# Kernel tuning notes

Measured on AMD Instinct MI355X. Metric: run time of the kernel, lower is better.

The kernel has to match this reference:

```python
import jax, jax.numpy as jnp
import numpy as np

B, T, TM = 4, 1024, 1500
D_MODEL, D_FFN, H, D_HEAD, D_MEM = 1024, 4096, 16, 64, 1024
EPS = 1e-5


def layernorm(x, g):
    m = jnp.mean(x, axis=-1, keepdims=True)
    xc = x - m
    v = jnp.mean(xc * xc, axis=-1, keepdims=True)
    return xc * jax.lax.rsqrt(v + EPS) * g


def setup_inputs() -> dict:
    key = jax.random.key(0)
    ks = jax.random.split(key, 12)
    s = lambda fan_in: 1.0 / np.sqrt(fan_in)
    return {
        "x": jax.random.normal(ks[0], (B, T, D_MODEL), jnp.float32),
        "encoder_output": jax.random.normal(ks[1], (B, TM, D_MEM), jnp.float32),
        "encoder_mask": jax.random.randint(ks[2], (B, TM), 0, 2).astype(bool),
        "w_qkv": jax.random.normal(ks[3], (D_MODEL, 3 * H * D_HEAD), jnp.float32) * s(D_MODEL),
        "w_o_sa": jax.random.normal(ks[4], (H * D_HEAD, D_MODEL), jnp.float32) * s(H * D_HEAD),
        "w_q": jax.random.normal(ks[5], (D_MODEL, H * D_HEAD), jnp.float32) * s(D_MODEL),
        "w_kv": jax.random.normal(ks[6], (D_MEM, 2 * H * D_HEAD), jnp.float32) * s(D_MEM),
        "w_o_xa": jax.random.normal(ks[7], (H * D_HEAD, D_MODEL), jnp.float32) * s(H * D_HEAD),
        "w_ff1": jax.random.normal(ks[8], (D_MODEL, D_FFN), jnp.float32) * s(D_MODEL),
        "w_ff2": jax.random.normal(ks[9], (D_FFN, D_MODEL), jnp.float32) * s(D_FFN),
        "g_sa": jnp.ones((D_MODEL,), jnp.float32),
        "g_xaq": jnp.ones((D_MODEL,), jnp.float32),
        "g_xam": jnp.ones((D_MEM,), jnp.float32),
        "g_ff": jnp.ones((D_MODEL,), jnp.float32),
    }


def reference(x, encoder_output, encoder_mask, w_qkv, w_o_sa, w_q, w_kv, w_o_xa,
              w_ff1, w_ff2, g_sa, g_xaq, g_xam, g_ff):
    b, t, _ = x.shape
    scale = D_HEAD ** -0.5

    # ---- causal self-attention ----
    residual = x
    xn = layernorm(x, g_sa)
    qkv = (xn @ w_qkv).reshape(b, t, 3, H, D_HEAD)
    q, k, v = qkv[:, :, 0], qkv[:, :, 1], qkv[:, :, 2]  # (B,T,H,D)
    scores = jnp.einsum('bqhd,bkhd->bhqk', q, k) * scale
    causal = jnp.tril(jnp.ones((t, t), x.dtype))
    scores = scores + (1.0 - causal) * -1e9
    attn = jax.nn.softmax(scores, axis=-1)
    sa = jnp.einsum('bhqk,bkhd->bqhd', attn, v).reshape(b, t, H * D_HEAD)
    x = residual + sa @ w_o_sa

    # ---- cross-attention ----
    residual = x
    qn = layernorm(x, g_xaq)
    mn = layernorm(encoder_output, g_xam)
    tq, tm = t, mn.shape[1]
    qx = (qn @ w_q).reshape(b, tq, H, D_HEAD)
    kvx = (mn @ w_kv).reshape(b, tm, 2, H, D_HEAD)
    kx, vx = kvx[:, :, 0], kvx[:, :, 1]
    xs = jnp.einsum('bqhd,bkhd->bhqk', qx, kx) * scale
    xs = jnp.where(encoder_mask[:, None, None, :], xs, -jnp.inf)
    xattn = jax.nn.softmax(xs, axis=-1)
    xa = jnp.einsum('bhqk,bkhd->bqhd', xattn, vx).reshape(b, tq, H * D_HEAD)
    x = residual + xa @ w_o_xa

    # ---- pointwise FFN (kernel_size=1 conv == linear) ----
    residual = x
    h = layernorm(x, g_ff)
    h = jax.nn.gelu(h @ w_ff1, approximate=True) @ w_ff2
    x = residual + h
    return (x, k, v)
```

## Files before the change

kernel.cpp:

```cpp
#include <hip/hip_runtime.h>
#include <hip/hip_bf16.h>
#include <cstdint>
#include <cstddef>


typedef __attribute__((ext_vector_type(4))) float f32x4;
typedef __attribute__((ext_vector_type(8))) short s8v;
typedef __attribute__((ext_vector_type(2))) unsigned uint2v;

#define DEVI __device__ __forceinline__

DEVI short f2bf(float f) {
  union { float f; unsigned u; } x; x.f = f;
  unsigned r = x.u + 0x7fffu + ((x.u >> 16) & 1u);
  return (short)(r >> 16);
}
DEVI unsigned cvtpk_bf2(float lo, float hi) {
  unsigned r;
  asm("v_cvt_pk_bf16_f32 %0, %1, %2" : "=v"(r) : "v"(lo), "v"(hi));
  return r;
}
DEVI float fexp2(float x) {
  float r;
  asm("v_exp_f32 %0, %1" : "=v"(r) : "v"(x));
  return r;
}
DEVI float fmax3(float a, float b, float c) {
  float r;
  asm("v_max3_f32 %0, %1, %2, %3" : "=v"(r) : "v"(a), "v"(b), "v"(c));
  return r;
}
DEVI float bpermf(int srclane, float v) {
  union { float f; int i; } x; x.f = v;
  x.i = __builtin_amdgcn_ds_bpermute(srclane << 2, x.i);
  return x.f;
}
DEVI void gload_lds16(const void* g, void* l) {
  __builtin_amdgcn_global_load_lds((const __attribute__((address_space(1))) void*)g,
                                   (__attribute__((address_space(3))) void*)l,
                                   16, 0, 0);
}

DEVI void xcd_swizzle(int& bx, int& by) {
  int gx = gridDim.x, gy = gridDim.y;
  int nxy = gx * gy, chunk = nxy >> 3;
  int orig = blockIdx.y * gx + blockIdx.x;
  int gid = (orig & 7) * chunk + (orig >> 3);
  int full = gy << 3, nfull = gx >> 3, lim = nfull * full;
  if (gid < lim) {
    int band = gid / full, r = gid - band * full;
    bx = (band << 3) + (r & 7);
    by = r >> 3;
  } else {
    int r = gid - lim, w = gx - (nfull << 3);
    bx = (nfull << 3) + r % w;
    by = r / w;
  }
}

__global__ __launch_bounds__(256) void k_prep(
    const float* __restrict__ wqkv, const float* __restrict__ wosa,
    const float* __restrict__ wq,   const float* __restrict__ wkv,
    const float* __restrict__ woxa, const float* __restrict__ wff1,
    const float* __restrict__ wff2,
    short* __restrict__ wqkv_t, short* __restrict__ wosa_t,
    short* __restrict__ wq_t,   short* __restrict__ wkv_t,
    short* __restrict__ woxa_t, short* __restrict__ wff1_t,
    short* __restrict__ wff2_t,
    const int* __restrict__ mask, unsigned long long* __restrict__ mbits) {
  int id = blockIdx.x;
  const float* w; short* wt; int K, N, tx, r;
  if (id < 3072)       { w = wqkv; wt = wqkv_t; K = 1024; N = 3072; tx = 96;  r = id; }
  else if (id < 4096)  { w = wosa; wt = wosa_t; K = 1024; N = 1024; tx = 32;  r = id - 3072; }
  else if (id < 5120)  { w = wq;   wt = wq_t;   K = 1024; N = 1024; tx = 32;  r = id - 4096; }
  else if (id < 7168)  { w = wkv;  wt = wkv_t;  K = 1024; N = 2048; tx = 64;  r = id - 5120; }
  else if (id < 8192)  { w = woxa; wt = woxa_t; K = 1024; N = 1024; tx = 32;  r = id - 7168; }
  else if (id < 12288) { w = wff1; wt = wff1_t; K = 1024; N = 4096; tx = 128; r = id - 8192; }
  else if (id < 16384) { w = wff2; wt = wff2_t; K = 4096; N = 1024; tx = 32;  r = id - 12288; }
  else {
    int t = threadIdx.x;
    if (t < 96) {
      int b = t / 24, wd = t % 24;
      unsigned long long v = 0;
      const int* mb = mask + (size_t)b * 1500;
      for (int j = 0; j < 64; j++) {
        int k = wd * 64 + j;
        if (k < 1500 && mb[k]) v |= (1ull << j);
      }
      mbits[b * 24 + wd] = v;
    }
    return;
  }
  __shared__ float tile[32][33];
  int n0 = (r % tx) * 32, k0 = (r / tx) * 32;
  int t = threadIdx.x;
  int row = t >> 3, c4 = (t & 7) * 4;
  *(f32x4*)&tile[row][c4] = *(const f32x4*)(w + (size_t)(k0 + row) * N + n0 + c4);
  __syncthreads();
  float v0 = tile[c4 + 0][row], v1 = tile[c4 + 1][row];
  float v2 = tile[c4 + 2][row], v3 = tile[c4 + 3][row];
  uint2v o = {cvtpk_bf2(v0, v1), cvtpk_bf2(v2, v3)};
  *(uint2v*)(wt + (size_t)(n0 + row) * K + k0 + c4) = o;
}

__global__ __launch_bounds__(256) void k_vtrans(
    const short* __restrict__ src, int srs, int coff,
    short* __restrict__ dst, int T, int Tp) {
  __shared__ short tile[32][72];
  int bh = blockIdx.y, b = bh >> 4, h = bh & 15;
  int t0 = blockIdx.x * 32;
  const short* sB = src + (size_t)b * T * srs + coff + h * 64;
  short* dB = dst + (size_t)bh * 64 * Tp;
  int t = threadIdx.x;
  int r = t >> 3, c = (t & 7) * 8;
  int tr = t0 + r; if (tr > T - 1) tr = T - 1;
  *(s8v*)&tile[r][c] = *(const s8v*)(sB + (size_t)tr * srs + c);
  __syncthreads();
  int d = t & 63, ch = t >> 6;
  s8v o;
#pragma unroll
  for (int j = 0; j < 8; j++) o[j] = tile[ch * 8 + j][d];
  *(s8v*)(dB + (size_t)d * Tp + t0 + ch * 8) = o;
}

__global__ __launch_bounds__(256) void k_ln2(
    const float* __restrict__ x, const float* __restrict__ gx,
    short* __restrict__ ox,
    const float* __restrict__ e, const float* __restrict__ ge,
    short* __restrict__ oe) {
  int id = blockIdx.x;
  const float* src; const float* g; short* dst; int row;
  if (id < 4096) { src = x; g = gx; dst = ox; row = id; }
  else           { src = e; g = ge; dst = oe; row = id - 4096; }
  const float* xr = src + (size_t)row * 1024;
  int t = threadIdx.x, wid = t >> 6, lane = t & 63;
  f32x4 v = ((const f32x4*)xr)[t];
  float s = v[0] + v[1] + v[2] + v[3];
#pragma unroll
  for (int m = 32; m >= 1; m >>= 1) s += __shfl_xor(s, m);
  __shared__ float red[4];
  if (lane == 0) red[wid] = s;
  __syncthreads();
  float mean = (red[0] + red[1] + red[2] + red[3]) * (1.f / 1024.f);
  float q = 0.f;
#pragma unroll
  for (int i = 0; i < 4; i++) { v[i] -= mean; q += v[i] * v[i]; }
#pragma unroll
  for (int m = 32; m >= 1; m >>= 1) q += __shfl_xor(q, m);
  __syncthreads();
  if (lane == 0) red[wid] = q;
  __syncthreads();
  float var = (red[0] + red[1] + red[2] + red[3]) * (1.f / 1024.f);
  float rs = rsqrtf(var + 1e-5f);
  f32x4 gv = ((const f32x4*)g)[t];
  uint2v w = {cvtpk_bf2(v[0] * rs * gv[0], v[1] * rs * gv[1]),
              cvtpk_bf2(v[2] * rs * gv[2], v[3] * rs * gv[3])};
  *(uint2v*)(dst + (size_t)row * 1024 + t * 4) = w;
}

__global__ __launch_bounds__(256) void k_ln(
    const float* __restrict__ x, const float* __restrict__ g,
    short* __restrict__ out) {
  int row = blockIdx.x;
  const float* xr = x + (size_t)row * 1024;
  int t = threadIdx.x, wid = t >> 6, lane = t & 63;
  f32x4 v = ((const f32x4*)xr)[t];
  float s = v[0] + v[1] + v[2] + v[3];
#pragma unroll
  for (int m = 32; m >= 1; m >>= 1) s += __shfl_xor(s, m);
  __shared__ float red[4];
  if (lane == 0) red[wid] = s;
  __syncthreads();
  float mean = (red[0] + red[1] + red[2] + red[3]) * (1.f / 1024.f);
  float q = 0.f;
#pragma unroll
  for (int i = 0; i < 4; i++) { v[i] -= mean; q += v[i] * v[i]; }
#pragma unroll
  for (int m = 32; m >= 1; m >>= 1) q += __shfl_xor(q, m);
  __syncthreads();
  if (lane == 0) red[wid] = q;
  __syncthreads();
  float var = (red[0] + red[1] + red[2] + red[3]) * (1.f / 1024.f);
  float rs = rsqrtf(var + 1e-5f);
  f32x4 gv = ((const f32x4*)g)[t];
  uint2v w = {cvtpk_bf2(v[0] * rs * gv[0], v[1] * rs * gv[1]),
              cvtpk_bf2(v[2] * rs * gv[2], v[3] * rs * gv[3])};
  *(uint2v*)(out + (size_t)row * 1024 + t * 4) = w;
}

template <bool GELU_, bool F32OUT, bool BF16OUT, bool KV, bool SPLIT>
__global__ __launch_bounds__(512) void k_gemm4(
    const short* __restrict__ A, const short* __restrict__ Bt,
    float* __restrict__ Cf, short* __restrict__ Cb,
    float* __restrict__ okv, int M, int N, int K, int lda, int ldb) {
  __shared__ short As[128 * 64];
  __shared__ short Bs[256 * 64];
  if (SPLIT) {
    int z = blockIdx.z;
    A += (size_t)z * K;
    Bt += (size_t)z * K;
    if (F32OUT) Cf += (size_t)z * (size_t)M * N;
  }

  int bx, by;
  xcd_swizzle(bx, by);
  int am = bx * 128, bn = by * 256;

  int t = threadIdx.x, wid = t >> 6, lane = t & 63;
  int la = lane & 15, lb = lane >> 4;
  int wr = wid >> 2, wc = wid & 3;

  const short* gpA[2]; const short* gpB[4];
  int dofA[2], dofB[4];
#pragma unroll
  for (int l = 0; l < 2; l++) {
    int c = l * 512 + t;
    int row = c >> 3, g = c & 7;
    int ar = am + row; if (ar > M - 1) ar = M - 1;
    gpA[l] = A + (size_t)ar * lda + ((g ^ (row & 7)) << 3);
    dofA[l] = (l * 512 + wid * 64) * 8;
  }
#pragma unroll
  for (int l = 0; l < 4; l++) {
    int c = l * 512 + t;
    int row = c >> 3, g = c & 7;
    gpB[l] = Bt + (size_t)(bn + row) * ldb + ((g ^ (row & 7)) << 3);
    dofB[l] = (l * 512 + wid * 64) * 8;
  }

  int aOff[4], bOff[4];
#pragma unroll
  for (int m = 0; m < 4; m++) {
    int r = wr * 64 + m * 16 + la;
    aOff[m] = r * 64 + ((lb ^ (r & 7)) << 3);
  }
#pragma unroll
  for (int n = 0; n < 4; n++) {
    int r = wc * 64 + n * 16 + la;
    bOff[n] = r * 64 + ((lb ^ (r & 7)) << 3);
  }

  f32x4 acc[4][4];
#pragma unroll
  for (int m = 0; m < 4; m++)
#pragma unroll
    for (int n = 0; n < 4; n++) acc[m][n] = (f32x4){0.f, 0.f, 0.f, 0.f};

  int nk = K >> 6;
  for (int ks = 0; ks < nk; ++ks) {
#pragma unroll
    for (int l = 0; l < 2; l++) { gload_lds16(gpA[l], As + dofA[l]); gpA[l] += 64; }
#pragma unroll
    for (int l = 0; l < 4; l++) { gload_lds16(gpB[l], Bs + dofB[l]); gpB[l] += 64; }
    __syncthreads();
#pragma unroll
    for (int kk = 0; kk < 2; kk++) {
      s8v af[4], bfg[4];
#pragma unroll
      for (int m = 0; m < 4; m++)
        af[m] = *(const s8v*)(As + (aOff[m] ^ (kk << 5)));
#pragma unroll
      for (int n = 0; n < 4; n++)
        bfg[n] = *(const s8v*)(Bs + (bOff[n] ^ (kk << 5)));
#pragma unroll
      for (int m = 0; m < 4; m++)
#pragma unroll
        for (int n = 0; n < 4; n++)
          acc[m][n] = __builtin_amdgcn_mfma_f32_16x16x32_bf16(af[m], bfg[n], acc[m][n], 0, 0, 0);
    }
    __syncthreads();
  }

#pragma unroll
  for (int m = 0; m < 4; m++) {
    int rb = am + wr * 64 + m * 16 + lb * 4;
#pragma unroll
    for (int n = 0; n < 4; n++) {
      int col = bn + wc * 64 + n * 16 + la;
#pragma unroll
      for (int j = 0; j < 4; j++) {
        int r = rb + j;
        if (r < M) {
          float v = acc[m][n][j];
          if (GELU_) {
            float u = v;
            float y = 0.7978845608f * u * (1.f + 0.044715f * u * u);
            float e = fexp2(fminf(y * 2.88539008f, 80.f));
            float th = (e - 1.f) * __builtin_amdgcn_rcpf(e + 1.f);
            v = 0.5f * u * (1.f + th);
          }
          if (F32OUT) Cf[(size_t)r * N + col] = v;
          if (BF16OUT) Cb[(size_t)r * N + col] = f2bf(v);
          if (KV) {
            if (col >= 2048)
              okv[(size_t)4096 * 1024 + (size_t)r * 1024 + (col - 2048)] = v;
            else if (col >= 1024)
              okv[(size_t)r * 1024 + (col - 1024)] = v;
          }
        }
      }
    }
  }
}

template <bool RES, bool F32OUT, bool BF16OUT>
__global__ __launch_bounds__(256) void k_gemm5(
    const short* __restrict__ A, const short* __restrict__ Bt,
    float* __restrict__ Cf, short* __restrict__ Cb,
    const float* __restrict__ res, int M, int N, int K, int lda, int ldb) {
  __shared__ short As[128 * 64];
  __shared__ short Bs[64 * 64];

  int bx, by;
  xcd_swizzle(bx, by);
  int am = bx * 128, bn = by * 64;

  int t = threadIdx.x, wid = t >> 6, lane = t & 63;
  int la = lane & 15, lb = lane >> 4;
  int wr = wid >> 1, wc = wid & 1;

  const short* gpA[4]; const short* gpB[2];
  int dofA[4], dofB[2];
#pragma unroll
  for (int l = 0; l < 4; l++) {
    int cl = l * 256 + t;
    int row = cl >> 3, g = cl & 7;
    int ar = am + row; if (ar > M - 1) ar = M - 1;
    gpA[l] = A + (size_t)ar * lda + ((g ^ (row & 7)) << 3);
    dofA[l] = (l * 256 + wid * 64) * 8;
  }
#pragma unroll
  for (int l = 0; l < 2; l++) {
    int cl = l * 256 + t;
    int row = cl >> 3, g = cl & 7;
    gpB[l] = Bt + (size_t)(bn + row) * ldb + ((g ^ (row & 7)) << 3);
    dofB[l] = (l * 256 + wid * 64) * 8;
  }

  int aOff[4], bOff[2];
#pragma unroll
  for (int m = 0; m < 4; m++) {
    int r = wr * 64 + m * 16 + la;
    aOff[m] = r * 64 + ((lb ^ (r & 7)) << 3);
  }
#pragma unroll
  for (int n = 0; n < 2; n++) {
    int r = wc * 32 + n * 16 + la;
    bOff[n] = r * 64 + ((lb ^ (r & 7)) << 3);
  }

  f32x4 acc[4][2];
#pragma unroll
  for (int m = 0; m < 4; m++)
#pragma unroll
    for (int n = 0; n < 2; n++) acc[m][n] = (f32x4){0.f, 0.f, 0.f, 0.f};

  int nk = K >> 6;
  for (int ks = 0; ks < nk; ++ks) {
#pragma unroll
    for (int l = 0; l < 4; l++) { gload_lds16(gpA[l], As + dofA[l]); gpA[l] += 64; }
#pragma unroll
    for (int l = 0; l < 2; l++) { gload_lds16(gpB[l], Bs + dofB[l]); gpB[l] += 64; }
    __syncthreads();
#pragma unroll
    for (int kk = 0; kk < 2; kk++) {
      s8v af[4], bfg[2];
#pragma unroll
      for (int m = 0; m < 4; m++)
        af[m] = *(const s8v*)(As + (aOff[m] ^ (kk << 5)));
#pragma unroll
      for (int n = 0; n < 2; n++)
        bfg[n] = *(const s8v*)(Bs + (bOff[n] ^ (kk << 5)));
#pragma unroll
      for (int m = 0; m < 4; m++)
#pragma unroll
        for (int n = 0; n < 2; n++)
          acc[m][n] = __builtin_amdgcn_mfma_f32_16x16x32_bf16(af[m], bfg[n], acc[m][n], 0, 0, 0);
    }
    __syncthreads();
  }

#pragma unroll
  for (int m = 0; m < 4; m++) {
    int rb = am + wr * 64 + m * 16 + lb * 4;
#pragma unroll
    for (int n = 0; n < 2; n++) {
      int col = bn + wc * 32 + n * 16 + la;
#pragma unroll
      for (int j = 0; j < 4; j++) {
        int r = rb + j;
        if (r < M) {
          float v = acc[m][n][j];
          if (RES) v += res[(size_t)r * N + col];
          if (F32OUT) Cf[(size_t)r * N + col] = v;
          if (BF16OUT) Cb[(size_t)r * N + col] = f2bf(v);
        }
      }
    }
  }
}

__global__ __launch_bounds__(256) void k_red4(
    const f32x4* __restrict__ p, const f32x4* __restrict__ res,
    float* __restrict__ outf, int n) {
  int i = blockIdx.x * 256 + threadIdx.x;
  f32x4 v = res[i] + ((p[i] + p[i + (size_t)n]) +
                      (p[i + 2 * (size_t)n] + p[i + 3 * (size_t)n]));
  ((f32x4*)outf)[i] = v;
}

template <bool CAUSAL>
__global__ __launch_bounds__(512) void k_attn4(
    const short* __restrict__ qbuf, int qrs,
    const short* __restrict__ kbuf, int krs,
    const short* __restrict__ vT, int vts,
    short* __restrict__ obuf, int ors,
    const unsigned long long* __restrict__ mbits, int mwords,
    int Tq, int Tk, float scale) {
  __shared__ short Ks[64 * 64];
  __shared__ short Vs[64 * 64];
  __shared__ short Ps[8 * 1024];
  int lid = blockIdx.y * gridDim.x + blockIdx.x;
  int rest = lid >> 3;
  int bh = (lid & 7) * 8 + (rest & 7);
  int qsel = rest >> 3;
  int st = CAUSAL ? (7 - qsel) : qsel;
  int b = bh >> 4, h = bh & 15;
  int t = threadIdx.x, wid = t >> 6, lane = t & 63;
  int la = lane & 15, lb = lane >> 4;
  float lscale = scale * 1.44269504f;

  const short* qB = qbuf + (size_t)b * Tq * qrs + h * 64;
  const short* kB = kbuf + (size_t)b * Tk * krs + h * 64;
  const short* vB = vT + (size_t)bh * 64 * vts;
  char* Pw = (char*)(Ps + wid * 1024);

  int sr = t >> 3, scol = (t & 7) * 8;
  int swz = sr * 64 + (scol ^ ((sr & 7) << 3));

  int q0 = st * 128 + wid * 16;
  int nkt = CAUSAL ? 2 * st + 2 : (Tk + 63) >> 6;
  int lastkt = CAUSAL ? (q0 >> 6) : nkt - 1;

  s8v qf[2];
#pragma unroll
  for (int kk = 0; kk < 2; kk++)
    qf[kk] = *(const s8v*)(qB + (size_t)(q0 + la) * qrs + kk * 32 + lb * 8);

  f32x4 accO[4];
#pragma unroll
  for (int n = 0; n < 4; n++) accO[n] = (f32x4){0.f, 0.f, 0.f, 0.f};
  float m = -1e30f, l = 0.f;

  s8v krg, vrg;
  {
    int tk = sr; if (tk > Tk - 1) tk = Tk - 1;
    krg = *(const s8v*)(kB + (size_t)tk * krs + scol);
    vrg = *(const s8v*)(vB + (size_t)sr * vts + scol);
  }

  for (int kt = 0; kt < nkt; kt++) {
    int kb0 = kt << 6;
    __syncthreads();
    *(s8v*)&Ks[swz] = krg;
    *(s8v*)&Vs[swz] = vrg;
    __syncthreads();
    if (kt + 1 < nkt) {
      int kb = kb0 + 64;
      int tk = kb + sr; if (tk > Tk - 1) tk = Tk - 1;
      krg = *(const s8v*)(kB + (size_t)tk * krs + scol);
      vrg = *(const s8v*)(vB + (size_t)sr * vts + kb + scol);
    }
    if (kt > lastkt) continue;

    bool needMask;
    unsigned long long wm = ~0ull;
    if (CAUSAL) {
      needMask = (kt == lastkt);
    } else {
      wm = mbits[(size_t)b * mwords + kt];
      needMask = (wm != ~0ull);
    }

    float sc[4][4];
    __builtin_amdgcn_s_setprio(1);
#pragma unroll
    for (int n = 0; n < 4; n++) {
      f32x4 a = (f32x4){0.f, 0.f, 0.f, 0.f};
#pragma unroll
      for (int kk = 0; kk < 2; kk++) {
        s8v kf = *(const s8v*)&Ks[(n * 16 + la) * 64 +
                                  ((kk * 32 + lb * 8) ^ ((la & 7) << 3))];
        a = __builtin_amdgcn_mfma_f32_16x16x32_bf16(kf, qf[kk], a, 0, 0, 0);
      }
      if (needMask) {
#pragma unroll
        for (int j = 0; j < 4; j++) {
          int ki = n * 16 + lb * 4 + j;
          bool ok = CAUSAL ? (kb0 + ki <= q0 + la) : (((wm >> ki) & 1ull) != 0);
          sc[n][j] = ok ? a[j] : -1e30f;
        }
      } else {
#pragma unroll
        for (int j = 0; j < 4; j++) sc[n][j] = a[j];
      }
    }
    __builtin_amdgcn_s_setprio(0);

    float rn[4];
#pragma unroll
    for (int n = 0; n < 4; n++)
      rn[n] = fmaxf(fmax3(sc[n][0], sc[n][1], sc[n][2]), sc[n][3]);
    float tm = fmaxf(fmax3(rn[0], rn[1], rn[2]), rn[3]);
    tm = fmaxf(tm, __shfl_xor(tm, 16));
    tm = fmaxf(tm, __shfl_xor(tm, 32));
    tm = fmaxf(tm * lscale, -1e4f);

    bool skip = __all(tm - m <= 10.f);
    float alpha = 1.f;
    if (!skip) {
      float mn_ = fmaxf(m, tm);
      alpha = fexp2(m - mn_);
      m = mn_;
    }
    float nm = -m;

    unsigned W[4][2];
    float ps = 0.f;
#pragma unroll
    for (int n = 0; n < 4; n++) {
      float p0 = fexp2(__builtin_fmaf(sc[n][0], lscale, nm));
      float p1 = fexp2(__builtin_fmaf(sc[n][1], lscale, nm));
      float p2 = fexp2(__builtin_fmaf(sc[n][2], lscale, nm));
      float p3 = fexp2(__builtin_fmaf(sc[n][3], lscale, nm));
      ps += (p0 + p1) + (p2 + p3);
      W[n][0] = cvtpk_bf2(p0, p1);
      W[n][1] = cvtpk_bf2(p2, p3);
    }
    ps += __shfl_xor(ps, 16);
    ps += __shfl_xor(ps, 32);
    l = l * alpha + ps;

    if (!skip) {
#pragma unroll
      for (int j = 0; j < 4; j++) {
        float aj = bpermf(lb * 20 + j, alpha);
#pragma unroll
        for (int n = 0; n < 4; n++) accO[n][j] *= aj;
      }
    }

#pragma unroll
    for (int n = 0; n < 4; n++) {
      uint2v w2 = {W[n][0], W[n][1]};
      *(uint2v*)(Pw + ((la * 128 + n * 32 + lb * 8) ^ ((la & 7) << 4))) = w2;
    }
    __builtin_amdgcn_s_setprio(1);
#pragma unroll
    for (int kk = 0; kk < 2; kk++) {
      s8v pa = *(const s8v*)(Pw + ((la * 128 + kk * 64 + lb * 16) ^ ((la & 7) << 4)));
#pragma unroll
      for (int n = 0; n < 4; n++) {
        s8v vf = *(const s8v*)&Vs[(n * 16 + la) * 64 +
                                  ((kk * 32 + lb * 8) ^ ((la & 7) << 3))];
        accO[n] = __builtin_amdgcn_mfma_f32_16x16x32_bf16(pa, vf, accO[n], 0, 0, 0);
      }
    }
    __builtin_amdgcn_s_setprio(0);
  }

#pragma unroll
  for (int j = 0; j < 4; j++) {
    float lj = bpermf(lb * 20 + j, l);
    float inv = 1.f / lj;
    int r = q0 + lb * 4 + j;
#pragma unroll
    for (int n = 0; n < 4; n++)
      obuf[(size_t)(b * Tq + r) * ors + h * 64 + n * 16 + la] = f2bf(accO[n][j] * inv);
  }
}

extern "C" void kernel_launch(void* const* d_in, const int* in_sizes, int n_in,
                              void* d_out, int out_size, void* d_ws, size_t ws_size,
                              hipStream_t stream) {
  (void)in_sizes; (void)n_in; (void)out_size; (void)ws_size;
  const float* x      = (const float*)d_in[0];
  const float* enc    = (const float*)d_in[1];
  const int*   mask   = (const int*)d_in[2];
  const float* w_qkv  = (const float*)d_in[3];
  const float* w_o_sa = (const float*)d_in[4];
  const float* w_q    = (const float*)d_in[5];
  const float* w_kv   = (const float*)d_in[6];
  const float* w_o_xa = (const float*)d_in[7];
  const float* w_ff1  = (const float*)d_in[8];
  const float* w_ff2  = (const float*)d_in[9];
  const float* g_sa   = (const float*)d_in[10];
  const float* g_xaq  = (const float*)d_in[11];
  const float* g_xam  = (const float*)d_in[12];
  const float* g_ff   = (const float*)d_in[13];

  float* out_x = (float*)d_out;
  float* out_k = out_x + (size_t)4096 * 1024;

  char* ws = (char*)d_ws;
  size_t off = 0;
  auto alloc = [&](size_t bytes) -> void* {
    void* p = ws + off;
    off += (bytes + 255) & ~(size_t)255;
    return p;
  };
  short* wqkv_t = (short*)alloc((size_t)3072 * 1024 * 2);
  short* wosa_t = (short*)alloc((size_t)1024 * 1024 * 2);
  short* wq_t   = (short*)alloc((size_t)1024 * 1024 * 2);
  short* wkv_t  = (short*)alloc((size_t)2048 * 1024 * 2);
  short* woxa_t = (short*)alloc((size_t)1024 * 1024 * 2);
  short* wff1_t = (short*)alloc((size_t)4096 * 1024 * 2);
  short* wff2_t = (short*)alloc((size_t)1024 * 4096 * 2);
  short* xn     = (short*)alloc((size_t)4096 * 1024 * 2);
  short* qkv_b  = (short*)alloc((size_t)4096 * 3072 * 2);
  short* sa_b   = (short*)alloc((size_t)4096 * 1024 * 2);
  float* x1     = (float*)alloc((size_t)4096 * 1024 * 4);
  short* qn     = (short*)alloc((size_t)4096 * 1024 * 2);
  short* mn     = (short*)alloc((size_t)6000 * 1024 * 2);
  short* qx_b   = (short*)alloc((size_t)4096 * 1024 * 2);
  short* kvx_b  = (short*)alloc((size_t)6000 * 2048 * 2);
  short* xa_b   = (short*)alloc((size_t)4096 * 1024 * 2);
  float* x2     = (float*)alloc((size_t)4096 * 1024 * 4);
  short* hn     = (short*)alloc((size_t)4096 * 1024 * 2);
  short* h1     = (short*)alloc((size_t)4096 * 4096 * 2);
  unsigned long long* mbits = (unsigned long long*)alloc(4 * 24 * 8);

  short* vTsa = xn;
  short* vTxa = h1;
  float* partQ = (float*)qkv_b;
  const int NRED = 1048576;

  k_prep<<<16385, 256, 0, stream>>>(
      w_qkv, w_o_sa, w_q, w_kv, w_o_xa, w_ff1, w_ff2,
      wqkv_t, wosa_t, wq_t, wkv_t, woxa_t, wff1_t, wff2_t, mask, mbits);
  k_ln2<<<10096, 256, 0, stream>>>(x, g_sa, xn, enc, g_xam, mn);

  k_gemm4<false, false, true, true, false><<<dim3(32, 12), 512, 0, stream>>>(
      xn, wqkv_t, nullptr, qkv_b, out_k, 4096, 3072, 1024, 1024, 1024);
  k_vtrans<<<dim3(32, 64), 256, 0, stream>>>(qkv_b, 3072, 2048, vTsa, 1024, 1024);
  k_attn4<true><<<dim3(8, 64), 512, 0, stream>>>(
      qkv_b, 3072, qkv_b + 1024, 3072, vTsa, 1024,
      sa_b, 1024, nullptr, 0, 1024, 1024, 0.125f);
  k_gemm5<true, true, false><<<dim3(32, 16), 256, 0, stream>>>(
      sa_b, wosa_t, x1, nullptr, x, 4096, 1024, 1024, 1024, 1024);
  k_ln<<<4096, 256, 0, stream>>>(x1, g_xaq, qn);

  k_gemm5<false, false, true><<<dim3(32, 16), 256, 0, stream>>>(
      qn, wq_t, nullptr, qx_b, nullptr, 4096, 1024, 1024, 1024, 1024);
  k_gemm4<false, false, true, false, false><<<dim3(47, 8), 512, 0, stream>>>(
      mn, wkv_t, nullptr, kvx_b, nullptr, 6000, 2048, 1024, 1024, 1024);
  k_vtrans<<<dim3(48, 64), 256, 0, stream>>>(kvx_b, 2048, 1024, vTxa, 1500, 1536);
  k_attn4<false><<<dim3(8, 64), 512, 0, stream>>>(
      qx_b, 1024, kvx_b, 2048, vTxa, 1536,
      xa_b, 1024, mbits, 24, 1024, 1500, 0.125f);
  k_gemm5<true, true, false><<<dim3(32, 16), 256, 0, stream>>>(
      xa_b, woxa_t, x2, nullptr, x1, 4096, 1024, 1024, 1024, 1024);
  k_ln<<<4096, 256, 0, stream>>>(x2, g_ff, hn);

  k_gemm4<true, false, true, false, false><<<dim3(32, 16), 512, 0, stream>>>(
      hn, wff1_t, nullptr, h1, nullptr, 4096, 4096, 1024, 1024, 1024);
  k_gemm4<false, true, false, false, true><<<dim3(32, 4, 4), 512, 0, stream>>>(
      h1, wff2_t, partQ, nullptr, nullptr, 4096, 1024, 1024, 4096, 4096);
  k_red4<<<4096, 256, 0, stream>>>(
      (const f32x4*)partQ, (const f32x4*)x2, out_x, NRED);
}
```

Measured before the change: 384.2 us.

## Process 128-key superblocks per iteration in attention kernel to halve barriers

The attention kernel now stages two 64-key K/V tiles per loop iteration, computing scores for 128 keys before a single online-softmax max/rescale step. This halves the number of __syncthreads pairs and softmax reductions per key range and prefetches two tiles at once. The cost is doubled LDS for K/V, more registers for scores and prefetch buffers, and possible reads past Tk for the V tile in the cross-attention case, which could lower occupancy.

```diff
diff --git a/kernel.cpp b/kernel.cpp
--- a/kernel.cpp
+++ b/kernel.cpp
@@ -417,8 +417,10 @@
     short* __restrict__ obuf, int ors,
     const unsigned long long* __restrict__ mbits, int mwords,
     int Tq, int Tk, float scale) {
-  __shared__ short Ks[64 * 64];
-  __shared__ short Vs[64 * 64];
+  __shared__ short Ks0[64 * 64];
+  __shared__ short Ks1[64 * 64];
+  __shared__ short Vs0[64 * 64];
+  __shared__ short Vs1[64 * 64];
   __shared__ short Ps[8 * 1024];
   int lid = blockIdx.y * gridDim.x + blockIdx.x;
   int rest = lid >> 3;
@@ -439,8 +441,8 @@
   int swz = sr * 64 + (scol ^ ((sr & 7) << 3));
 
   int q0 = st * 128 + wid * 16;
-  int nkt = CAUSAL ? 2 * st + 2 : (Tk + 63) >> 6;
-  int lastkt = CAUSAL ? (q0 >> 6) : nkt - 1;
+  int lastkt = CAUSAL ? (q0 >> 6) : 0x7fffffff;
+  int nss = CAUSAL ? (st + 1) : ((Tk + 127) >> 7);
 
   s8v qf[2];
 #pragma unroll
@@ -452,66 +454,86 @@
   for (int n = 0; n < 4; n++) accO[n] = (f32x4){0.f, 0.f, 0.f, 0.f};
   float m = -1e30f, l = 0.f;
 
-  s8v krg, vrg;
+  s8v krg0, krg1, vrg0, vrg1;
   {
-    int tk = sr; if (tk > Tk - 1) tk = Tk - 1;
-    krg = *(const s8v*)(kB + (size_t)tk * krs + scol);
-    vrg = *(const s8v*)(vB + (size_t)sr * vts + scol);
-  }
-
-  for (int kt = 0; kt < nkt; kt++) {
-    int kb0 = kt << 6;
+    int tk0 = sr; if (tk0 > Tk - 1) tk0 = Tk - 1;
+    int tk1 = 64 + sr; if (tk1 > Tk - 1) tk1 = Tk - 1;
+    krg0 = *(const s8v*)(kB + (size_t)tk0 * krs + scol);
+    krg1 = *(const s8v*)(kB + (size_t)tk1 * krs + scol);
+    vrg0 = *(const s8v*)(vB + (size_t)sr * vts + scol);
+    vrg1 = *(const s8v*)(vB + (size_t)sr * vts + 64 + scol);
+  }
+
+  for (int ss = 0; ss < nss; ss++) {
     __syncthreads();
-    *(s8v*)&Ks[swz] = krg;
-    *(s8v*)&Vs[swz] = vrg;
+    *(s8v*)&Ks0[swz] = krg0;
+    *(s8v*)&Ks1[swz] = krg1;
+    *(s8v*)&Vs0[swz] = vrg0;
+    *(s8v*)&Vs1[swz] = vrg1;
     __syncthreads();
-    if (kt + 1 < nkt) {
-      int kb = kb0 + 64;
-      int tk = kb + sr; if (tk > Tk - 1) tk = Tk - 1;
-      krg = *(const s8v*)(kB + (size_t)tk * krs + scol);
-      vrg = *(const s8v*)(vB + (size_t)sr * vts + kb + scol);
-    }
-    if (kt > lastkt) continue;
-
-    bool needMask;
-    unsigned long long wm = ~0ull;
-    if (CAUSAL) {
-      needMask = (kt == lastkt);
-    } else {
-      wm = mbits[(size_t)b * mwords + kt];
-      needMask = (wm != ~0ull);
-    }
-
-    float sc[4][4];
-    __builtin_amdgcn_s_setprio(1);
-#pragma unroll
-    for (int n = 0; n < 4; n++) {
-      f32x4 a = (f32x4){0.f, 0.f, 0.f, 0.f};
-#pragma unroll
-      for (int kk = 0; kk < 2; kk++) {
-        s8v kf = *(const s8v*)&Ks[(n * 16 + la) * 64 +
-                                  ((kk * 32 + lb * 8) ^ ((la & 7) << 3))];
-        a = __builtin_amdgcn_mfma_f32_16x16x32_bf16(kf, qf[kk], a, 0, 0, 0);
-      }
-      if (needMask) {
-#pragma unroll
-        for (int j = 0; j < 4; j++) {
-          int ki = n * 16 + lb * 4 + j;
-          bool ok = CAUSAL ? (kb0 + ki <= q0 + la) : (((wm >> ki) & 1ull) != 0);
-          sc[n][j] = ok ? a[j] : -1e30f;
+    if (ss + 1 < nss) {
+      int kb = (ss + 1) << 7;
+      int tk0 = kb + sr; if (tk0 > Tk - 1) tk0 = Tk - 1;
+      int tk1 = kb + 64 + sr; if (tk1 > Tk - 1) tk1 = Tk - 1;
+      krg0 = *(const s8v*)(kB + (size_t)tk0 * krs + scol);
+      krg1 = *(const s8v*)(kB + (size_t)tk1 * krs + scol);
+      vrg0 = *(const s8v*)(vB + (size_t)sr * vts + kb + scol);
+      vrg1 = *(const s8v*)(vB + (size_t)sr * vts + kb + 64 + scol);
+    }
+
+    float sc[8][4];
+    bool act1 = !CAUSAL || (2 * ss + 1 <= lastkt);
+#pragma unroll
+    for (int hf = 0; hf < 2; hf++) {
+      const short* Kh = hf ? Ks1 : Ks0;
+      int kt64 = 2 * ss + hf;
+      if (hf == 1 && !act1) {
+#pragma unroll
+        for (int n = 0; n < 4; n++)
+#pragma unroll
+          for (int j = 0; j < 4; j++) sc[4 + n][j] = -1e30f;
+        continue;
+      }
+      bool needMask;
+      unsigned long long wm = ~0ull;
+      if (CAUSAL) {
+        needMask = (kt64 == lastkt);
+      } else {
+        wm = mbits[(size_t)b * mwords + kt64];
+        needMask = (wm != ~0ull);
+      }
+      __builtin_amdgcn_s_setprio(1);
+#pragma unroll
+      for (int n = 0; n < 4; n++) {
+        f32x4 a = (f32x4){0.f, 0.f, 0.f, 0.f};
+#pragma unroll
+        for (int kk = 0; kk < 2; kk++) {
+          s8v kf = *(const s8v*)&Kh[(n * 16 + la) * 64 +
+                                    ((kk * 32 + lb * 8) ^ ((la & 7) << 3))];
+          a = __builtin_amdgcn_mfma_f32_16x16x32_bf16(kf, qf[kk], a, 0, 0, 0);
         }
-      } else {
-#pragma unroll
-        for (int j = 0; j < 4; j++) sc[n][j] = a[j];
-      }
-    }
-    __builtin_amdgcn_s_setprio(0);
-
-    float rn[4];
-#pragma unroll
-    for (int n = 0; n < 4; n++)
+        if (needMask) {
+#pragma unroll
+          for (int j = 0; j < 4; j++) {
+            int ki = n * 16 + lb * 4 + j;
+            bool ok = CAUSAL ? ((kt64 << 6) + ki <= q0 + la)
+                             : (((wm >> ki) & 1ull) != 0);
+            sc[hf * 4 + n][j] = ok ? a[j] : -1e30f;
+          }
+        } else {
+#pragma unroll
+          for (int j = 0; j < 4; j++) sc[hf * 4 + n][j] = a[j];
+        }
+      }
+      __builtin_amdgcn_s_setprio(0);
+    }
+
+    float rn[8];
+#pragma unroll
+    for (int n = 0; n < 8; n++)
       rn[n] = fmaxf(fmax3(sc[n][0], sc[n][1], sc[n][2]), sc[n][3]);
-    float tm = fmaxf(fmax3(rn[0], rn[1], rn[2]), rn[3]);
+    float tm = fmax3(fmax3(rn[0], rn[1], rn[2]), fmax3(rn[3], rn[4], rn[5]),
+                     fmaxf(rn[6], rn[7]));
     tm = fmaxf(tm, __shfl_xor(tm, 16));
     tm = fmaxf(tm, __shfl_xor(tm, 32));
     tm = fmaxf(tm * lscale, -1e4f);
@@ -525,48 +547,52 @@
     }
     float nm = -m;
 
-    unsigned W[4][2];
+    if (!skip) {
+#pragma unroll
+      for (int j = 0; j < 4; j++) {
+        float aj = bpermf(lb * 20 + j, alpha);
+#pragma unroll
+        for (int n = 0; n < 4; n++) accO[n][j] *= aj;
+      }
+    }
+
     float ps = 0.f;
 #pragma unroll
-    for (int n = 0; n < 4; n++) {
-      float p0 = fexp2(__builtin_fmaf(sc[n][0], lscale, nm));
-      float p1 = fexp2(__builtin_fmaf(sc[n][1], lscale, nm));
-      float p2 = fexp2(__builtin_fmaf(sc[n][2], lscale, nm));
-      float p3 = fexp2(__builtin_fmaf(sc[n][3], lscale, nm));
-      ps += (p0 + p1) + (p2 + p3);
-      W[n][0] = cvtpk_bf2(p0, p1);
-      W[n][1] = cvtpk_bf2(p2, p3);
+    for (int hf = 0; hf < 2; hf++) {
+      if (hf == 1 && !act1) continue;
+      const short* Vh = hf ? Vs1 : Vs0;
+      unsigned W[4][2];
+#pragma unroll
+      for (int n = 0; n < 4; n++) {
+        float p0 = fexp2(__builtin_fmaf(sc[hf * 4 + n][0], lscale, nm));
+        float p1 = fexp2(__builtin_fmaf(sc[hf * 4 + n][1], lscale, nm));
+        float p2 = fexp2(__builtin_fmaf(sc[hf * 4 + n][2], lscale, nm));
+        float p3 = fexp2(__builtin_fmaf(sc[hf * 4 + n][3], lscale, nm));
+        ps += (p0 + p1) + (p2 + p3);
+        W[n][0] = cvtpk_bf2(p0, p1);
+        W[n][1] = cvtpk_bf2(p2, p3);
+      }
+#pragma unroll
+      for (int n = 0; n < 4; n++) {
+        uint2v w2 = {W[n][0], W[n][1]};
+        *(uint2v*)(Pw + ((la * 128 + n * 32 + lb * 8) ^ ((la & 7) << 4))) = w2;
+      }
+      __builtin_amdgcn_s_setprio(1);
+#pragma unroll
+      for (int kk = 0; kk < 2; kk++) {
+        s8v pa = *(const s8v*)(Pw + ((la * 128 + kk * 64 + lb * 16) ^ ((la & 7) << 4)));
+#pragma unroll
+        for (int n = 0; n < 4; n++) {
+          s8v vf = *(const s8v*)&Vh[(n * 16 + la) * 64 +
+                                    ((kk * 32 + lb * 8) ^ ((la & 7) << 3))];
+          accO[n] = __builtin_amdgcn_mfma_f32_16x16x32_bf16(pa, vf, accO[n], 0, 0, 0);
+        }
+      }
+      __builtin_amdgcn_s_setprio(0);
     }
     ps += __shfl_xor(ps, 16);
     ps += __shfl_xor(ps, 32);
     l = l * alpha + ps;
-
-    if (!skip) {
-#pragma unroll
-      for (int j = 0; j < 4; j++) {
-        float aj = bpermf(lb * 20 + j, alpha);
-#pragma unroll
-        for (int n = 0; n < 4; n++) accO[n][j] *= aj;
-      }
-    }
-
-#pragma unroll
-    for (int n = 0; n < 4; n++) {
-      uint2v w2 = {W[n][0], W[n][1]};
-      *(uint2v*)(Pw + ((la * 128 + n * 32 + lb * 8) ^ ((la & 7) << 4))) = w2;
-    }
-    __builtin_amdgcn_s_setprio(1);
-#pragma unroll
-    for (int kk = 0; kk < 2; kk++) {
-      s8v pa = *(const s8v*)(Pw + ((la * 128 + kk * 64 + lb * 16) ^ ((la & 7) << 4)));
-#pragma unroll
-      for (int n = 0; n < 4; n++) {
-        s8v vf = *(const s8v*)&Vs[(n * 16 + la) * 64 +
-                                  ((kk * 32 + lb * 8) ^ ((la & 7) << 3))];
-        accO[n] = __builtin_amdgcn_mfma_f32_16x16x32_bf16(pa, vf, accO[n], 0, 0, 0);
-      }
-    }
-    __builtin_amdgcn_s_setprio(0);
   }
 
 #pragma unroll
```

Result: slower. 397.3 us (+3.4%).
